# Kernel tuning notes

Measured on AMD Instinct MI355X. Metric: run time of the kernel, lower is better.

Reference implementation:

```python
import jax, jax.numpy as jnp
import numpy as np

EPS = 1e-6  # GLOBAL_EPS
D_QK = 192
ATTN_DIM = 768


def setup_inputs() -> dict:
    key = jax.random.key(0)
    ks = jax.random.split(key, 12)
    B, C, H, W = 16, 192, 56, 56
    d_qk, d_v = D_QK, 2 * D_QK
    attn_dim, inner = ATTN_DIM, d_v
    r = lambda k, s, sc=0.05: jax.random.normal(k, s, dtype=jnp.float32) * sc
    return {
        "x": jax.random.normal(ks[0], (B, C, H, W), dtype=jnp.float32),
        "proj_w": r(ks[1], (attn_dim, C)),          # 1x1 conv + BN folded
        "proj_b": r(ks[2], (attn_dim,)),
        "dwc_w": r(ks[3], (attn_dim, 1, 3, 3)),     # depthwise 3x3, BN folded
        "dwc_b": r(ks[4], (attn_dim,)),
        "g_w": r(ks[5], (inner, attn_dim)),          # ConvGate pointwise conv1d
        "g_b": r(ks[6], (inner,)),
        "an_w": 1.0 + r(ks[7], (inner,)),            # RMSNorm weight
        "sv": 1.0 + r(ks[8], (inner,)),              # Scale(inner, (1, inner, 1))
        "out_w": r(ks[9], (C, inner)),               # 1x1 conv + BN folded
        "out_b": r(ks[10], (C,)),
    }


def reference(x, proj_w, proj_b, dwc_w, dwc_b, g_w, g_b, an_w, sv, out_w, out_b):
    B, C, H, W = x.shape
    d_qk = D_QK
    # proj: ConvNorm 1x1 (conv + BN folded to affine)
    y = jnp.einsum("bchw,oc->bohw", x, proj_w) + proj_b[None, :, None, None]
    # dwc: RepConv depthwise 3x3 with residual (res=True)
    dw = jax.lax.conv_general_dilated(
        y, dwc_w, window_strides=(1, 1), padding="SAME",
        dimension_numbers=("NCHW", "OIHW", "NCHW"),
        feature_group_count=ATTN_DIM)
    y = dw + dwc_b[None, :, None, None] + y
    # flatten spatial -> tokens, split q/k/v along channels
    xs = y.reshape(B, ATTN_DIM, H * W)            # (B, attn_dim, N)
    q, k, v = xs[:, :d_qk], xs[:, d_qk:2 * d_qk], xs[:, 2 * d_qk:]
    # linear_attn: feature map = silu, scale = N**-0.5
    qf = jax.nn.silu(q)                            # (B, d_qk, N)
    kf = jax.nn.silu(k)
    N = H * W
    s = N ** -0.5
    # use_linear branch (N >> d): z = kT.mean(-2,True) @ q + eps ; attn = (v s)(kT s) q
    z = jnp.einsum("bd,bdn->bn", kf.mean(-1), qf)[:, None, :] + EPS  # (B, 1, N)
    vk = jnp.einsum("bvn,bdn->bvd", v * s, kf * s)  # (B, d_v, d_qk)
    attn = jnp.einsum("bvd,bdn->bvn", vk, qf) / z   # (B, d_v, N)
    # gate: pointwise conv1d on full projected features + sigmoid
    gate = jax.nn.sigmoid(jnp.einsum("bcn,oc->bon", xs, g_w) + g_b[None, :, None])
    attn = attn * gate
    # attn_norm (RMS over channels) + scale_v(v) residual
    rms = jnp.sqrt(jnp.mean(attn * attn, axis=1, keepdims=True) + EPS)
    attn = attn / rms * an_w[None, :, None] + v * sv[None, :, None]
    # out: ConvNorm 1x1 back to dim
    o = attn.reshape(B, -1, H, W)
    return jnp.einsum("bchw,oc->bohw", o, out_w) + out_b[None, :, None, None]
```

## Files before the change

### kernel.cpp

```cpp
#include <hip/hip_runtime.h>
#include <hip/hip_bf16.h>

typedef unsigned short u16;
typedef __attribute__((ext_vector_type(8))) short bf16x8;
typedef __attribute__((ext_vector_type(4))) float f32x4;

constexpr int B_ = 16, C_ = 192, H_ = 56, W_ = 56;
constexpr int N_ = H_ * W_;
constexpr int A_ = 768;
constexpr int Dq = 192;
constexpr int Vd = 384;
constexpr float EPSf = 1e-6f;

union U8 { bf16x8 v; u16 s[8]; unsigned u[4]; };

__device__ __forceinline__ float bits2f(u16 u) {
  return __uint_as_float(((unsigned)u) << 16);
}
__device__ __forceinline__ u16 f2bits(float f) {
  __hip_bfloat16 h = __float2bfloat16(f);
  u16 u;
  __builtin_memcpy(&u, &h, sizeof(u));
  return u;
}
__device__ __forceinline__ float silu_f(float v) { return v / (1.0f + __expf(-v)); }
__device__ __forceinline__ float sigm_f(float v) { return 1.0f / (1.0f + __expf(-v)); }

__device__ __forceinline__ f32x4 MFMA(bf16x8 a, bf16x8 b, f32x4 c) {
  return __builtin_amdgcn_mfma_f32_16x16x32_bf16(a, b, c, 0, 0, 0);
}
__device__ __forceinline__ int swz(int row) { return (row & 7) ^ ((row >> 3) & 7); }

__global__ __launch_bounds__(256) void k_prep(const float* __restrict__ pw,
                                              const float* __restrict__ gw,
                                              const float* __restrict__ ow,
                                              u16* __restrict__ pwb,
                                              u16* __restrict__ gwb,
                                              u16* __restrict__ owb,
                                              float* __restrict__ kfp) {
  const int bid = blockIdx.x;
  if (bid == 252) {
    for (int i = threadIdx.x; i < B_ * Dq; i += 256) kfp[i] = 0.f;
    return;
  }
  const size_t base = ((size_t)bid * 256 + threadIdx.x) * 8;
  const float* src;
  u16* dst;
  size_t off;
  if (bid < 72) { src = pw; dst = pwb; off = base; }
  else if (bid < 216) { src = gw; dst = gwb; off = base - 147456; }
  else { src = ow; dst = owb; off = base - 442368; }
  float4 v0 = *(const float4*)&src[off];
  float4 v1 = *(const float4*)&src[off + 4];
  U8 r;
  r.s[0] = f2bits(v0.x); r.s[1] = f2bits(v0.y); r.s[2] = f2bits(v0.z); r.s[3] = f2bits(v0.w);
  r.s[4] = f2bits(v1.x); r.s[5] = f2bits(v1.y); r.s[6] = f2bits(v1.z); r.s[7] = f2bits(v1.w);
  *(bf16x8*)&dst[off] = r.v;
}

__global__ __launch_bounds__(256) void k_proj(const float* __restrict__ x,
                                              const u16* __restrict__ pwb,
                                              const float* __restrict__ pb,
                                              u16* __restrict__ y0t) {
  const int n0 = blockIdx.x * 64;
  const int oy = blockIdx.y;
  const int b = blockIdx.z;
  __shared__ u16 Xt[64][200];
  __shared__ u16 Wa[256][32];
  const int t = threadIdx.x;
  const int lane = t & 63, wid = t >> 6;
  const int fr = lane & 15, fg = lane >> 4;

  {
    const int p = t & 31, co = t >> 5;
    const float* xb = x + (size_t)b * C_ * N_ + n0 + 2 * p;
#pragma unroll
    for (int rnd = 0; rnd < 3; ++rnd) {
      const int c0 = rnd * 64 + co * 8;
      float2 v[8];
#pragma unroll
      for (int i = 0; i < 8; ++i) v[i] = *(const float2*)&xb[(size_t)(c0 + i) * N_];
      U8 r0, r1;
#pragma unroll
      for (int i = 0; i < 8; ++i) { r0.s[i] = f2bits(v[i].x); r1.s[i] = f2bits(v[i].y); }
      *(bf16x8*)&Xt[2 * p][c0] = r0.v;
      *(bf16x8*)&Xt[2 * p + 1][c0] = r1.v;
    }
  }

  f32x4 acc[4][4];
#pragma unroll
  for (int mi = 0; mi < 4; ++mi)
#pragma unroll
    for (int ni = 0; ni < 4; ++ni) acc[mi][ni] = (f32x4){0.f, 0.f, 0.f, 0.f};

  const int orow_c = t >> 2, oct_c = t & 3;
  U8 wreg[4];
#pragma unroll
  for (int jj = 0; jj < 4; ++jj)
    wreg[jj].v = *(const bf16x8*)&pwb[(size_t)(oy * 256 + orow_c + 64 * jj) * C_ + oct_c * 8];

  for (int ks = 0; ks < 6; ++ks) {
    __syncthreads();
#pragma unroll
    for (int jj = 0; jj < 4; ++jj) {
      const int orow = orow_c + 64 * jj;
      const int sw = (orow >> 1) & 3;
      *(bf16x8*)&Wa[orow][(oct_c ^ sw) * 8] = wreg[jj].v;
    }
    __syncthreads();
    if (ks < 5) {
#pragma unroll
      for (int jj = 0; jj < 4; ++jj)
        wreg[jj].v = *(const bf16x8*)&pwb[(size_t)(oy * 256 + orow_c + 64 * jj) * C_ +
                                          (ks + 1) * 32 + oct_c * 8];
    }
    bf16x8 bfrag[4];
#pragma unroll
    for (int ni = 0; ni < 4; ++ni)
      bfrag[ni] = *(const bf16x8*)&Xt[ni * 16 + fr][ks * 32 + fg * 8];
    __builtin_amdgcn_s_setprio(1);
#pragma unroll
    for (int mi = 0; mi < 4; ++mi) {
      const int ar = wid * 64 + mi * 16 + fr;
      bf16x8 a = *(const bf16x8*)&Wa[ar][(fg ^ ((ar >> 1) & 3)) * 8];
#pragma unroll
      for (int ni = 0; ni < 4; ++ni) acc[mi][ni] = MFMA(a, bfrag[ni], acc[mi][ni]);
    }
    __builtin_amdgcn_s_setprio(0);
  }
#pragma unroll
  for (int mi = 0; mi < 4; ++mi) {
    const int o4 = oy * 256 + wid * 64 + mi * 16 + fg * 4;
    const float b0 = pb[o4], b1 = pb[o4 + 1], b2 = pb[o4 + 2], b3 = pb[o4 + 3];
#pragma unroll
    for (int ni = 0; ni < 4; ++ni) {
      const int n = n0 + ni * 16 + fr;
      ushort4 pk;
      pk.x = f2bits(acc[mi][ni][0] + b0);
      pk.y = f2bits(acc[mi][ni][1] + b1);
      pk.z = f2bits(acc[mi][ni][2] + b2);
      pk.w = f2bits(acc[mi][ni][3] + b3);
      *(ushort4*)&y0t[((size_t)b * N_ + n) * A_ + o4] = pk;
    }
  }
}

__global__ __launch_bounds__(256) void k_dwc(const u16* __restrict__ y0t,
                                             const float* __restrict__ cw,
                                             const float* __restrict__ cb,
                                             u16* __restrict__ yt,
                                             float* __restrict__ kfp) {
  const int pid = blockIdx.x;
  const int L = (pid & 7) * 336 + (pid >> 3);
  const int h = L % 56, at = (L / 56) % 3, b = L / 168;
  const int t = threadIdx.x;
  const int a = at * 256 + (t & 31) * 8;
  const int ws0 = (t >> 5) * 7;
  float w9[9][8];
  float bias[8];
#pragma unroll
  for (int j = 0; j < 8; ++j) {
    bias[j] = cb[a + j];
#pragma unroll
    for (int k = 0; k < 9; ++k) w9[k][j] = cw[(a + j) * 9 + k];
  }
  const u16* src = y0t + (size_t)b * N_ * A_ + a;
  u16* dst = yt + (size_t)b * N_ * A_ + a;
  const bool hok0 = h > 0, hok2 = h < 55;

  U8 cm[3], cc[3], cp[3];
  auto zero8 = [](U8& x) { x.u[0] = x.u[1] = x.u[2] = x.u[3] = 0u; };
  auto loadcol = [&](U8 col[3], int w) {
    if ((unsigned)w < 56u) {
      if (hok0) col[0].v = *(const bf16x8*)&src[(size_t)((h - 1) * 56 + w) * A_];
      else zero8(col[0]);
      col[1].v = *(const bf16x8*)&src[(size_t)(h * 56 + w) * A_];
      if (hok2) col[2].v = *(const bf16x8*)&src[(size_t)((h + 1) * 56 + w) * A_];
      else zero8(col[2]);
    } else {
      zero8(col[0]); zero8(col[1]); zero8(col[2]);
    }
  };
  loadcol(cm, ws0 - 1);
  loadcol(cc, ws0);

  float kacc[8] = {0.f, 0.f, 0.f, 0.f, 0.f, 0.f, 0.f, 0.f};
#pragma unroll
  for (int i = 0; i < 7; ++i) {
    const int w = ws0 + i;
    loadcol(cp, w + 1);
    U8 o;
#pragma unroll
    for (int j = 0; j < 8; ++j) {
      float s = bias[j] + bits2f(cc[1].s[j]);
      s = fmaf(w9[0][j], bits2f(cm[0].s[j]), s);
      s = fmaf(w9[1][j], bits2f(cc[0].s[j]), s);
      s = fmaf(w9[2][j], bits2f(cp[0].s[j]), s);
      s = fmaf(w9[3][j], bits2f(cm[1].s[j]), s);
      s = fmaf(w9[4][j], bits2f(cc[1].s[j]), s);
      s = fmaf(w9[5][j], bits2f(cp[1].s[j]), s);
      s = fmaf(w9[6][j], bits2f(cm[2].s[j]), s);
      s = fmaf(w9[7][j], bits2f(cc[2].s[j]), s);
      s = fmaf(w9[8][j], bits2f(cp[2].s[j]), s);
      o.s[j] = f2bits(s);
      const int ch = a + j;
      if (ch >= 192 && ch < 384) kacc[j] += silu_f(s);
    }
    *(bf16x8*)&dst[(size_t)(h * 56 + w) * A_] = o.v;
#pragma unroll
    for (int r = 0; r < 3; ++r) { cm[r] = cc[r]; cc[r] = cp[r]; }
  }

  __shared__ float red[8][256];
  if (at < 2) {
    const int cbase = (t & 31) * 8, wl = t >> 5;
#pragma unroll
    for (int j = 0; j < 8; ++j) red[wl][cbase + j] = kacc[j];
    __syncthreads();
    float s = 0.f;
#pragma unroll
    for (int i = 0; i < 8; ++i) s += red[i][t];
    const int ac = at * 256 + t;
    if (ac >= 192 && ac < 384) atomicAdd(&kfp[b * Dq + (ac - 192)], s);
  }
}

__global__ __launch_bounds__(256) void k_z(const u16* __restrict__ yt,
                                           const float* __restrict__ kfp,
                                           float* __restrict__ zinv) {
  const int b = blockIdx.y;
  const int n = blockIdx.x * 256 + threadIdx.x;
  __shared__ float kf[192];
  if (threadIdx.x < 192)
    kf[threadIdx.x] = kfp[b * Dq + threadIdx.x] * (1.0f / (float)N_);
  __syncthreads();
  if (n < N_) {
    const u16* p = yt + ((size_t)b * N_ + n) * A_;
    float z = 0;
#pragma unroll
    for (int j = 0; j < 24; ++j) {
      U8 u;
      u.v = *(const bf16x8*)&p[j * 8];
#pragma unroll
      for (int i = 0; i < 8; ++i) z = fmaf(kf[j * 8 + i], silu_f(bits2f(u.s[i])), z);
    }
    zinv[(size_t)b * N_ + n] = 1.0f / (z + EPSf);
  }
}

__global__ __launch_bounds__(256) void k_vk(const u16* __restrict__ yt,
                                            float* __restrict__ vkpart) {
  const int pid = blockIdx.x;
  const int L = (pid & 7) * 42 + (pid >> 3);
  const int ns = L % 7;
  const int vblk = (L / 7) % 3;
  const int b = L / 21;
  const int t = threadIdx.x;
  const int lane = t & 63, wid = t >> 6;
  const int fr = lane & 15, fg = lane >> 4;
  const int vbase = (wid >> 1) * 64, dbase = (wid & 1) * 96;

  __shared__ u16 T[320 * 64];
  unsigned* T32 = (unsigned*)T;

  const int oct0 = t & 7;
  const int pair = (t >> 3) & 31;
  const int nb0 = ns * 448;

  U8 pre[5][2];
  auto load_pre = [&](int n0) {
    const int n = nb0 + n0 + pair * 2;
#pragma unroll
    for (int j = 0; j < 5; ++j) {
      const int oct = oct0 + 8 * j;
      const u16* srcp;
      if (j < 3)
        srcp = yt + ((size_t)b * N_ + n) * A_ + 192 + oct * 8;
      else
        srcp = yt + ((size_t)b * N_ + n) * A_ + 384 + vblk * 128 + (oct - 24) * 8;
      pre[j][0].v = *(const bf16x8*)srcp;
      pre[j][1].v = *(const bf16x8*)(srcp + A_);
      if (j < 3) {
#pragma unroll
        for (int i = 0; i < 8; ++i) {
          pre[j][0].s[i] = f2bits(silu_f(bits2f(pre[j][0].s[i])));
          pre[j][1].s[i] = f2bits(silu_f(bits2f(pre[j][1].s[i])));
        }
      }
    }
  };

  f32x4 acc[4][6];
#pragma unroll
  for (int mi = 0; mi < 4; ++mi)
#pragma unroll
    for (int ni = 0; ni < 6; ++ni) acc[mi][ni] = (f32x4){0.f, 0.f, 0.f, 0.f};

  load_pre(0);
  for (int s = 0; s < 7; ++s) {
    __syncthreads();
#pragma unroll
    for (int j = 0; j < 5; ++j) {
      const int rowb = (oct0 + 8 * j) * 8;
#pragma unroll
      for (int i = 0; i < 8; ++i) {
        const int row = rowb + i;
        const int sw = swz(row);
        const unsigned val =
            ((unsigned)pre[j][0].s[i] & 0xffffu) | (((unsigned)pre[j][1].s[i]) << 16);
        T32[row * 32 + (pair ^ (sw << 2))] = val;
      }
    }
    __syncthreads();
    if (s < 6) load_pre((s + 1) * 64);
    __builtin_amdgcn_s_setprio(1);
#pragma unroll
    for (int kf2 = 0; kf2 < 2; ++kf2) {
      bf16x8 bfrag[6];
#pragma unroll
      for (int ni = 0; ni < 6; ++ni) {
        const int row = dbase + ni * 16 + fr;
        bfrag[ni] = *(const bf16x8*)&T[row * 64 + ((kf2 * 32 + fg * 8) ^ (swz(row) << 3))];
      }
#pragma unroll
      for (int mi = 0; mi < 4; ++mi) {
        const int row = 192 + vbase + mi * 16 + fr;
        bf16x8 a = *(const bf16x8*)&T[row * 64 + ((kf2 * 32 + fg * 8) ^ (swz(row) << 3))];
#pragma unroll
        for (int ni = 0; ni < 6; ++ni) acc[mi][ni] = MFMA(a, bfrag[ni], acc[mi][ni]);
      }
    }
    __builtin_amdgcn_s_setprio(0);
  }
  float* base = vkpart + (((size_t)ns * 16 + b) * 3 + vblk) * (128 * 192);
#pragma unroll
  for (int mi = 0; mi < 4; ++mi)
#pragma unroll
    for (int ni = 0; ni < 6; ++ni) {
      const int v = vbase + mi * 16 + fg * 4;
      const int d = dbase + ni * 16 + fr;
      float* o = base + (size_t)v * 192 + d;
      o[0] = acc[mi][ni][0];
      o[192] = acc[mi][ni][1];
      o[384] = acc[mi][ni][2];
      o[576] = acc[mi][ni][3];
    }
}

__global__ __launch_bounds__(256) void k_vkred(const float* __restrict__ vkpart,
                                               u16* __restrict__ vkb) {
  const size_t e = ((size_t)blockIdx.x * 256 + threadIdx.x) * 8;
  constexpr size_t NSSTRIDE = (size_t)16 * 3 * 128 * 192;
  float4 s0 = {0, 0, 0, 0}, s1 = {0, 0, 0, 0};
#pragma unroll
  for (int ns = 0; ns < 7; ++ns) {
    float4 a0 = *(const float4*)&vkpart[ns * NSSTRIDE + e];
    float4 a1 = *(const float4*)&vkpart[ns * NSSTRIDE + e + 4];
    s0.x += a0.x; s0.y += a0.y; s0.z += a0.z; s0.w += a0.w;
    s1.x += a1.x; s1.y += a1.y; s1.z += a1.z; s1.w += a1.w;
  }
  const float sc = 1.0f / (float)N_;
  U8 r;
  r.s[0] = f2bits(s0.x * sc); r.s[1] = f2bits(s0.y * sc);
  r.s[2] = f2bits(s0.z * sc); r.s[3] = f2bits(s0.w * sc);
  r.s[4] = f2bits(s1.x * sc); r.s[5] = f2bits(s1.y * sc);
  r.s[6] = f2bits(s1.z * sc); r.s[7] = f2bits(s1.w * sc);
  *(bf16x8*)&vkb[e] = r.v;
}

__global__ __launch_bounds__(256) void k_gateattn(const u16* __restrict__ yt,
                                                  const float* __restrict__ zinv,
                                                  const u16* __restrict__ vkb,
                                                  const u16* __restrict__ gwb,
                                                  const float* __restrict__ gb,
                                                  u16* __restrict__ attnt) {
  const int pid = blockIdx.x;
  const int L = (pid & 7) * 196 + (pid >> 3);
  const int vh = L & 1;
  const int n0 = ((L >> 1) % 49) * 64;
  const int b = L / 98;
  const int t = threadIdx.x;
  const int lane = t & 63, wid = t >> 6, wm = wid >> 1, wn = wid & 1;
  const int fr = lane & 15, fg = lane >> 4;
  __shared__ u16 T[2][256 * 64];
  __shared__ float zl[64];
  if (t < 64) zl[t] = zinv[(size_t)b * N_ + n0 + t];
  const u16* yb = yt + ((size_t)b * N_ + n0) * A_;
  const u16* wb0 = vkb + ((size_t)b * Vd + vh * 192) * 192;
  const u16* wb1 = gwb + (size_t)(vh * 192) * A_;

  const int oct = t & 7, rowb = t >> 3;
  U8 pre[8];
  auto loadPre = [&](int nit) {
    if (nit < 3) {
      const int ks = nit * 64;
#pragma unroll
      for (int j = 0; j < 6; ++j)
        pre[j].v = *(const bf16x8*)&wb0[(size_t)(rowb + 32 * j) * 192 + ks + oct * 8];
#pragma unroll
      for (int j = 6; j < 8; ++j)
        pre[j].v = *(const bf16x8*)&yb[(size_t)(rowb + 32 * (j - 6)) * A_ + ks + oct * 8];
    } else {
      const int ks = (nit - 3) * 64;
#pragma unroll
      for (int j = 0; j < 6; ++j)
        pre[j].v = *(const bf16x8*)&wb1[(size_t)(rowb + 32 * j) * A_ + ks + oct * 8];
#pragma unroll
      for (int j = 6; j < 8; ++j)
        pre[j].v = *(const bf16x8*)&yb[(size_t)(rowb + 32 * (j - 6)) * A_ + ks + oct * 8];
    }
  };
  auto writeStage = [&](int nit, int buf) {
    const bool sl = (nit < 3);
    u16* Tb = &T[buf][0];
#pragma unroll
    for (int j = 0; j < 8; ++j) {
      const int r = rowb + 32 * j;
      U8 w = pre[j];
      if (sl && j >= 6) {
#pragma unroll
        for (int i = 0; i < 8; ++i) w.s[i] = f2bits(silu_f(bits2f(w.s[i])));
      }
      *(bf16x8*)&Tb[r * 64 + ((oct * 8) ^ (swz(r) << 3))] = w.v;
    }
  };

  f32x4 acc[6][2];
#pragma unroll
  for (int mi = 0; mi < 6; ++mi)
#pragma unroll
    for (int ni = 0; ni < 2; ++ni) acc[mi][ni] = (f32x4){0.f, 0.f, 0.f, 0.f};
  uint2 pp[6][2];

  loadPre(0);
  writeStage(0, 0);
  loadPre(1);
  __syncthreads();

  for (int it = 0; it < 15; ++it) {
    const int cur = it & 1;
    if (it < 14) writeStage(it + 1, cur ^ 1);
    if (it < 13) loadPre(it + 2);
    const u16* Tb = &T[cur][0];
    __builtin_amdgcn_s_setprio(1);
#pragma unroll
    for (int kf2 = 0; kf2 < 2; ++kf2) {
      bf16x8 bfr[2];
#pragma unroll
      for (int ni = 0; ni < 2; ++ni) {
        const int row = 192 + wn * 32 + ni * 16 + fr;
        bfr[ni] = *(const bf16x8*)&Tb[row * 64 + ((kf2 * 32 + fg * 8) ^ (swz(row) << 3))];
      }
#pragma unroll
      for (int mi = 0; mi < 6; ++mi) {
        const int row = wm * 96 + mi * 16 + fr;
        bf16x8 a = *(const bf16x8*)&Tb[row * 64 + ((kf2 * 32 + fg * 8) ^ (swz(row) << 3))];
        acc[mi][0] = MFMA(a, bfr[0], acc[mi][0]);
        acc[mi][1] = MFMA(a, bfr[1], acc[mi][1]);
      }
    }
    __builtin_amdgcn_s_setprio(0);
    if (it == 2) {
#pragma unroll
      for (int mi = 0; mi < 6; ++mi)
#pragma unroll
        for (int ni = 0; ni < 2; ++ni) {
          const float z = zl[wn * 32 + ni * 16 + fr];
          unsigned a0 = ((unsigned)f2bits(acc[mi][ni][0] * z) & 0xffffu) |
                        (((unsigned)f2bits(acc[mi][ni][1] * z) & 0xffffu) << 16);
          unsigned a1 = ((unsigned)f2bits(acc[mi][ni][2] * z) & 0xffffu) |
                        (((unsigned)f2bits(acc[mi][ni][3] * z) & 0xffffu) << 16);
          pp[mi][ni] = make_uint2(a0, a1);
          acc[mi][ni] = (f32x4){0.f, 0.f, 0.f, 0.f};
        }
    }
    __syncthreads();
  }

#pragma unroll
  for (int mi = 0; mi < 6; ++mi) {
    const int vb = vh * 192 + wm * 96 + mi * 16 + fg * 4;
    const float g0 = gb[vb], g1 = gb[vb + 1], g2 = gb[vb + 2], g3 = gb[vb + 3];
#pragma unroll
    for (int ni = 0; ni < 2; ++ni) {
      const int n = n0 + wn * 32 + ni * 16 + fr;
      const uint2 p = pp[mi][ni];
      const float pv0 = bits2f((u16)(p.x & 0xffffu)), pv1 = bits2f((u16)(p.x >> 16));
      const float pv2 = bits2f((u16)(p.y & 0xffffu)), pv3 = bits2f((u16)(p.y >> 16));
      ushort4 o;
      o.x = f2bits(pv0 * sigm_f(acc[mi][ni][0] + g0));
      o.y = f2bits(pv1 * sigm_f(acc[mi][ni][1] + g1));
      o.z = f2bits(pv2 * sigm_f(acc[mi][ni][2] + g2));
      o.w = f2bits(pv3 * sigm_f(acc[mi][ni][3] + g3));
      *(ushort4*)&attnt[((size_t)b * N_ + n) * Vd + vb] = o;
    }
  }
}

__global__ __launch_bounds__(256) void k_out(const u16* __restrict__ attnt,
                                             const u16* __restrict__ yt,
                                             const u16* __restrict__ owb,
                                             const float* __restrict__ ob,
                                             const float* __restrict__ anw,
                                             const float* __restrict__ svw,
                                             float* __restrict__ out) {
  const int n0 = blockIdx.x * 64;
  const int b = blockIdx.y;
  __shared__ u16 T[256 * 64];
  __shared__ float anws[384], svws[384];
  __shared__ float red[64][4];
  __shared__ float rinv[64];
  const int t = threadIdx.x;
  const int lane = t & 63, wid = t >> 6, wm = wid >> 1, wn = wid & 1;
  const int fr = lane & 15, fg = lane >> 4;
  for (int i = t; i < 384; i += 256) {
    anws[i] = anw[i];
    svws[i] = svw[i];
  }
  {
    const int n = t >> 2, q = t & 3;
    const u16* ab = attnt + ((size_t)b * N_ + n0 + n) * Vd;
    float ss = 0.f;
#pragma unroll
    for (int i = 0; i < 4; ++i) {
      U8 u, u2, u3;
      u.v = *(const bf16x8*)&ab[(q + 4 * i) * 8 + 0];
      u2.v = *(const bf16x8*)&ab[(q + 4 * i) * 8 + 128];
      u3.v = *(const bf16x8*)&ab[(q + 4 * i) * 8 + 256];
#pragma unroll
      for (int k = 0; k < 8; ++k) {
        float f0 = bits2f(u.s[k]), f1 = bits2f(u2.s[k]), f2 = bits2f(u3.s[k]);
        ss = fmaf(f0, f0, ss);
        ss = fmaf(f1, f1, ss);
        ss = fmaf(f2, f2, ss);
      }
    }
    red[n][q] = ss;
  }
  __syncthreads();
  if (t < 64)
    rinv[t] = rsqrtf((red[t][0] + red[t][1] + red[t][2] + red[t][3]) * (1.0f / (float)Vd) + EPSf);

  const int oct = t & 7, rowb = t >> 3;
  U8 preW[6], preA[2], preV[2];
  auto loadPre = [&](int it) {
    const int ks = it * 64;
#pragma unroll
    for (int j = 0; j < 6; ++j)
      preW[j].v = *(const bf16x8*)&owb[(size_t)(rowb + 32 * j) * Vd + ks + oct * 8];
#pragma unroll
    for (int j = 0; j < 2; ++j) {
      const int n = rowb + 32 * j;
      preA[j].v = *(const bf16x8*)&attnt[((size_t)b * N_ + n0 + n) * Vd + ks + oct * 8];
      preV[j].v = *(const bf16x8*)&yt[((size_t)b * N_ + n0 + n) * A_ + 384 + ks + oct * 8];
    }
  };

  f32x4 acc[6][2];
#pragma unroll
  for (int mi = 0; mi < 6; ++mi)
#pragma unroll
    for (int ni = 0; ni < 2; ++ni) acc[mi][ni] = (f32x4){0.f, 0.f, 0.f, 0.f};

  loadPre(0);
  __syncthreads();
  for (int it = 0; it < 6; ++it) {
#pragma unroll
    for (int j = 0; j < 6; ++j) {
      const int r = rowb + 32 * j;
      *(bf16x8*)&T[r * 64 + ((oct * 8) ^ (swz(r) << 3))] = preW[j].v;
    }
#pragma unroll
    for (int j = 0; j < 2; ++j) {
      const int n = rowb + 32 * j;
      const int r = 192 + n;
      const float ri = rinv[n];
      const int col0 = it * 64 + oct * 8;
      U8 o;
#pragma unroll
      for (int k = 0; k < 8; ++k)
        o.s[k] = f2bits(bits2f(preA[j].s[k]) * ri * anws[col0 + k] +
                        bits2f(preV[j].s[k]) * svws[col0 + k]);
      *(bf16x8*)&T[r * 64 + ((oct * 8) ^ (swz(r) << 3))] = o.v;
    }
    __syncthreads();
    if (it < 5) loadPre(it + 1);
    __builtin_amdgcn_s_setprio(1);
#pragma unroll
    for (int kf2 = 0; kf2 < 2; ++kf2) {
      bf16x8 bfr[2];
#pragma unroll
      for (int ni = 0; ni < 2; ++ni) {
        const int row = 192 + wn * 32 + ni * 16 + fr;
        bfr[ni] = *(const bf16x8*)&T[row * 64 + ((kf2 * 32 + fg * 8) ^ (swz(row) << 3))];
      }
#pragma unroll
      for (int mi = 0; mi < 6; ++mi) {
        const int row = wm * 96 + mi * 16 + fr;
        bf16x8 a = *(const bf16x8*)&T[row * 64 + ((kf2 * 32 + fg * 8) ^ (swz(row) << 3))];
        acc[mi][0] = MFMA(a, bfr[0], acc[mi][0]);
        acc[mi][1] = MFMA(a, bfr[1], acc[mi][1]);
      }
    }
    __builtin_amdgcn_s_setprio(0);
    if (it < 5) __syncthreads();
  }
#pragma unroll
  for (int mi = 0; mi < 6; ++mi) {
    const int c = wm * 96 + mi * 16 + fg * 4;
    const float b0 = ob[c], b1 = ob[c + 1], b2 = ob[c + 2], b3 = ob[c + 3];
#pragma unroll
    for (int ni = 0; ni < 2; ++ni) {
      const int n = n0 + wn * 32 + ni * 16 + fr;
      float* o = out + ((size_t)b * C_ + c) * N_ + n;
      o[0 * N_] = acc[mi][ni][0] + b0;
      o[1 * N_] = acc[mi][ni][1] + b1;
      o[2 * N_] = acc[mi][ni][2] + b2;
      o[3 * N_] = acc[mi][ni][3] + b3;
    }
  }
}

extern "C" void kernel_launch(void* const* d_in, const int* in_sizes, int n_in,
                              void* d_out, int out_size, void* d_ws, size_t ws_size,
                              hipStream_t stream) {
  (void)in_sizes; (void)n_in; (void)out_size; (void)ws_size;
  const float* x = (const float*)d_in[0];
  const float* pw = (const float*)d_in[1];
  const float* pb = (const float*)d_in[2];
  const float* cw = (const float*)d_in[3];
  const float* cb = (const float*)d_in[4];
  const float* gw = (const float*)d_in[5];
  const float* gb = (const float*)d_in[6];
  const float* anw = (const float*)d_in[7];
  const float* svw = (const float*)d_in[8];
  const float* ow = (const float*)d_in[9];
  const float* ob = (const float*)d_in[10];
  float* out = (float*)d_out;

  char* ws = (char*)d_ws;
  const size_t szY = (size_t)B_ * N_ * A_ * 2;
  u16* y0t = (u16*)(ws);
  u16* attnt = (u16*)(ws);
  float* vkpart = (float*)(ws + 38535168);
  u16* vkb = (u16*)(ws + 71565312);
  u16* yt = (u16*)(ws + szY);
  char* ws2 = ws + 2 * szY;
  float* kfp = (float*)(ws2);
  float* zinv = (float*)(ws2 + 86016);
  u16* pwb = (u16*)(ws2 + 86016 + 200704);
  u16* gwb = (u16*)(ws2 + 86016 + 200704 + 294912);
  u16* owb = (u16*)(ws2 + 86016 + 200704 + 294912 + 589824);

  k_prep<<<dim3(253), 256, 0, stream>>>(pw, gw, ow, pwb, gwb, owb, kfp);
  k_proj<<<dim3(49, 3, 16), 256, 0, stream>>>(x, pwb, pb, y0t);
  k_dwc<<<dim3(2688), 256, 0, stream>>>(y0t, cw, cb, yt, kfp);
  k_z<<<dim3(13, 16), 256, 0, stream>>>(yt, kfp, zinv);
  k_vk<<<dim3(336), 256, 0, stream>>>(yt, vkpart);
  k_vkred<<<dim3(576), 256, 0, stream>>>(vkpart, vkb);
  k_gateattn<<<dim3(1568), 256, 0, stream>>>(yt, zinv, vkb, gwb, gb, attnt);
  k_out<<<dim3(49, 16), 256, 0, stream>>>(attnt, yt, owb, ob, anw, svw, out);
}
```

Measured before the change: 264.0 us.

## Fuse z normalizer into gate-attn staging and move RMS sum-of-squares into epilogue

Removes the separate k_z kernel by computing the per-token dot of mean silu(k) with silu(q) while the q tile is staged into shared memory in k_gateattn, reducing it with shuffles before the z scaling is needed. The sum of squares for the RMS norm is also accumulated in the k_gateattn epilogue and added to a global buffer with atomics, so k_out no longer rereads attn to compute it. This saves one launch and two passes over global data, but adds an extra barrier, redundant per-block z work (both v halves compute it), atomics, and a larger zero-init in k_prep. The sum of squares is now taken on unrounded fp32 values instead of the bf16-rounded ones.

```diff
diff --git a/kernel.cpp b/kernel.cpp
--- a/kernel.cpp
+++ b/kernel.cpp
@@ -37,10 +37,15 @@
                                               u16* __restrict__ pwb,
                                               u16* __restrict__ gwb,
                                               u16* __restrict__ owb,
-                                              float* __restrict__ kfp) {
+                                              float* __restrict__ kfp,
+                                              float* __restrict__ ssq) {
   const int bid = blockIdx.x;
   if (bid == 252) {
-    for (int i = threadIdx.x; i < B_ * Dq; i += 256) kfp[i] = 0.f;
+    const int tot = B_ * Dq + B_ * N_;
+    for (int i = threadIdx.x; i < tot; i += 256) {
+      if (i < B_ * Dq) kfp[i] = 0.f;
+      else ssq[i - B_ * Dq] = 0.f;
+    }
     return;
   }
   const size_t base = ((size_t)bid * 256 + threadIdx.x) * 8;
@@ -226,29 +231,6 @@
   }
 }
 
-__global__ __launch_bounds__(256) void k_z(const u16* __restrict__ yt,
-                                           const float* __restrict__ kfp,
-                                           float* __restrict__ zinv) {
-  const int b = blockIdx.y;
-  const int n = blockIdx.x * 256 + threadIdx.x;
-  __shared__ float kf[192];
-  if (threadIdx.x < 192)
-    kf[threadIdx.x] = kfp[b * Dq + threadIdx.x] * (1.0f / (float)N_);
-  __syncthreads();
-  if (n < N_) {
-    const u16* p = yt + ((size_t)b * N_ + n) * A_;
-    float z = 0;
-#pragma unroll
-    for (int j = 0; j < 24; ++j) {
-      U8 u;
-      u.v = *(const bf16x8*)&p[j * 8];
-#pragma unroll
-      for (int i = 0; i < 8; ++i) z = fmaf(kf[j * 8 + i], silu_f(bits2f(u.s[i])), z);
-    }
-    zinv[(size_t)b * N_ + n] = 1.0f / (z + EPSf);
-  }
-}
-
 __global__ __launch_bounds__(256) void k_vk(const u16* __restrict__ yt,
                                             float* __restrict__ vkpart) {
   const int pid = blockIdx.x;
@@ -370,11 +352,12 @@
 }
 
 __global__ __launch_bounds__(256) void k_gateattn(const u16* __restrict__ yt,
-                                                  const float* __restrict__ zinv,
+                                                  const float* __restrict__ kfp,
                                                   const u16* __restrict__ vkb,
                                                   const u16* __restrict__ gwb,
                                                   const float* __restrict__ gb,
-                                                  u16* __restrict__ attnt) {
+                                                  u16* __restrict__ attnt,
+                                                  float* __restrict__ ssq) {
   const int pid = blockIdx.x;
   const int L = (pid & 7) * 196 + (pid >> 3);
   const int vh = L & 1;
@@ -385,13 +368,15 @@
   const int fr = lane & 15, fg = lane >> 4;
   __shared__ u16 T[2][256 * 64];
   __shared__ float zl[64];
-  if (t < 64) zl[t] = zinv[(size_t)b * N_ + n0 + t];
+  __shared__ float kfs[192];
+  if (t < 192) kfs[t] = kfp[b * Dq + t] * (1.0f / (float)N_);
   const u16* yb = yt + ((size_t)b * N_ + n0) * A_;
   const u16* wb0 = vkb + ((size_t)b * Vd + vh * 192) * 192;
   const u16* wb1 = gwb + (size_t)(vh * 192) * A_;
 
   const int oct = t & 7, rowb = t >> 3;
   U8 pre[8];
+  float zp[2] = {0.f, 0.f};
   auto loadPre = [&](int nit) {
     if (nit < 3) {
       const int ks = nit * 64;
@@ -413,6 +398,7 @@
   };
   auto writeStage = [&](int nit, int buf) {
     const bool sl = (nit < 3);
+    const int kbase = nit * 64 + oct * 8;
     u16* Tb = &T[buf][0];
 #pragma unroll
     for (int j = 0; j < 8; ++j) {
@@ -420,7 +406,11 @@
       U8 w = pre[j];
       if (sl && j >= 6) {
 #pragma unroll
-        for (int i = 0; i < 8; ++i) w.s[i] = f2bits(silu_f(bits2f(w.s[i])));
+        for (int i = 0; i < 8; ++i) {
+          const float sv = silu_f(bits2f(w.s[i]));
+          zp[j - 6] = fmaf(kfs[kbase + i], sv, zp[j - 6]);
+          w.s[i] = f2bits(sv);
+        }
       }
       *(bf16x8*)&Tb[r * 64 + ((oct * 8) ^ (swz(r) << 3))] = w.v;
     }
@@ -434,6 +424,7 @@
   uint2 pp[6][2];
 
   loadPre(0);
+  __syncthreads();
   writeStage(0, 0);
   loadPre(1);
   __syncthreads();
@@ -441,6 +432,15 @@
   for (int it = 0; it < 15; ++it) {
     const int cur = it & 1;
     if (it < 14) writeStage(it + 1, cur ^ 1);
+    if (it == 1) {
+      float z0 = zp[0], z1 = zp[1];
+      z0 += __shfl_xor(z0, 1); z0 += __shfl_xor(z0, 2); z0 += __shfl_xor(z0, 4);
+      z1 += __shfl_xor(z1, 1); z1 += __shfl_xor(z1, 2); z1 += __shfl_xor(z1, 4);
+      if (oct == 0) {
+        zl[rowb] = 1.0f / (z0 + EPSf);
+        zl[rowb + 32] = 1.0f / (z1 + EPSf);
+      }
+    }
     if (it < 13) loadPre(it + 2);
     const u16* Tb = &T[cur][0];
     __builtin_amdgcn_s_setprio(1);
@@ -478,6 +478,7 @@
     __syncthreads();
   }
 
+  float ssqa[2] = {0.f, 0.f};
 #pragma unroll
   for (int mi = 0; mi < 6; ++mi) {
     const int vb = vh * 192 + wm * 96 + mi * 16 + fg * 4;
@@ -488,12 +489,27 @@
       const uint2 p = pp[mi][ni];
       const float pv0 = bits2f((u16)(p.x & 0xffffu)), pv1 = bits2f((u16)(p.x >> 16));
       const float pv2 = bits2f((u16)(p.y & 0xffffu)), pv3 = bits2f((u16)(p.y >> 16));
+      const float q0 = pv0 * sigm_f(acc[mi][ni][0] + g0);
+      const float q1 = pv1 * sigm_f(acc[mi][ni][1] + g1);
+      const float q2 = pv2 * sigm_f(acc[mi][ni][2] + g2);
+      const float q3 = pv3 * sigm_f(acc[mi][ni][3] + g3);
       ushort4 o;
-      o.x = f2bits(pv0 * sigm_f(acc[mi][ni][0] + g0));
-      o.y = f2bits(pv1 * sigm_f(acc[mi][ni][1] + g1));
-      o.z = f2bits(pv2 * sigm_f(acc[mi][ni][2] + g2));
-      o.w = f2bits(pv3 * sigm_f(acc[mi][ni][3] + g3));
+      o.x = f2bits(q0);
+      o.y = f2bits(q1);
+      o.z = f2bits(q2);
+      o.w = f2bits(q3);
       *(ushort4*)&attnt[((size_t)b * N_ + n) * Vd + vb] = o;
+      ssqa[ni] += q0 * q0 + q1 * q1 + q2 * q2 + q3 * q3;
+    }
+  }
+#pragma unroll
+  for (int ni = 0; ni < 2; ++ni) {
+    float ss = ssqa[ni];
+    ss += __shfl_xor(ss, 16);
+    ss += __shfl_xor(ss, 32);
+    if (fg == 0) {
+      const int n = n0 + wn * 32 + ni * 16 + fr;
+      atomicAdd(&ssq[(size_t)b * N_ + n], ss);
     }
   }
 }
@@ -504,12 +520,12 @@
                                              const float* __restrict__ ob,
                                              const float* __restrict__ anw,
                                              const float* __restrict__ svw,
+                                             const float* __restrict__ ssq,
                                              float* __restrict__ out) {
   const int n0 = blockIdx.x * 64;
   const int b = blockIdx.y;
   __shared__ u16 T[256 * 64];
   __shared__ float anws[384], svws[384];
-  __shared__ float red[64][4];
   __shared__ float rinv[64];
   const int t = threadIdx.x;
   const int lane = t & 63, wid = t >> 6, wm = wid >> 1, wn = wid & 1;
@@ -518,29 +534,8 @@
     anws[i] = anw[i];
     svws[i] = svw[i];
   }
-  {
-    const int n = t >> 2, q = t & 3;
-    const u16* ab = attnt + ((size_t)b * N_ + n0 + n) * Vd;
-    float ss = 0.f;
-#pragma unroll
-    for (int i = 0; i < 4; ++i) {
-      U8 u, u2, u3;
-      u.v = *(const bf16x8*)&ab[(q + 4 * i) * 8 + 0];
-      u2.v = *(const bf16x8*)&ab[(q + 4 * i) * 8 + 128];
-      u3.v = *(const bf16x8*)&ab[(q + 4 * i) * 8 + 256];
-#pragma unroll
-      for (int k = 0; k < 8; ++k) {
-        float f0 = bits2f(u.s[k]), f1 = bits2f(u2.s[k]), f2 = bits2f(u3.s[k]);
-        ss = fmaf(f0, f0, ss);
-        ss = fmaf(f1, f1, ss);
-        ss = fmaf(f2, f2, ss);
-      }
-    }
-    red[n][q] = ss;
-  }
-  __syncthreads();
   if (t < 64)
-    rinv[t] = rsqrtf((red[t][0] + red[t][1] + red[t][2] + red[t][3]) * (1.0f / (float)Vd) + EPSf);
+    rinv[t] = rsqrtf(ssq[(size_t)b * N_ + n0 + t] * (1.0f / (float)Vd) + EPSf);
 
   const int oct = t & 7, rowb = t >> 3;
   U8 preW[6], preA[2], preV[2];
@@ -648,17 +643,16 @@
   u16* yt = (u16*)(ws + szY);
   char* ws2 = ws + 2 * szY;
   float* kfp = (float*)(ws2);
-  float* zinv = (float*)(ws2 + 86016);
+  float* ssq = (float*)(ws2 + 86016);
   u16* pwb = (u16*)(ws2 + 86016 + 200704);
   u16* gwb = (u16*)(ws2 + 86016 + 200704 + 294912);
   u16* owb = (u16*)(ws2 + 86016 + 200704 + 294912 + 589824);
 
-  k_prep<<<dim3(253), 256, 0, stream>>>(pw, gw, ow, pwb, gwb, owb, kfp);
+  k_prep<<<dim3(253), 256, 0, stream>>>(pw, gw, ow, pwb, gwb, owb, kfp, ssq);
   k_proj<<<dim3(49, 3, 16), 256, 0, stream>>>(x, pwb, pb, y0t);
   k_dwc<<<dim3(2688), 256, 0, stream>>>(y0t, cw, cb, yt, kfp);
-  k_z<<<dim3(13, 16), 256, 0, stream>>>(yt, kfp, zinv);
   k_vk<<<dim3(336), 256, 0, stream>>>(yt, vkpart);
   k_vkred<<<dim3(576), 256, 0, stream>>>(vkpart, vkb);
-  k_gateattn<<<dim3(1568), 256, 0, stream>>>(yt, zinv, vkb, gwb, gb, attnt);
-  k_out<<<dim3(49, 16), 256, 0, stream>>>(attnt, yt, owb, ob, anw, svw, out);
-}
+  k_gateattn<<<dim3(1568), 256, 0, stream>>>(yt, kfp, vkb, gwb, gb, attnt, ssq);
+  k_out<<<dim3(49, 16), 256, 0, stream>>>(attnt, yt, owb, ob, anw, svw, ssq, out);
+}
```

Result: no change. 261.8 us, median of 2 (-0.8%).
